# Performance work log

Hardware: AMD Instinct MI355X
Metric: run time of the kernel (lower is better)

## Reference

```python
import jax, jax.numpy as jnp
import numpy as np

B, S, D, H = 4, 2048, 1024, 16
HD = D // H
FF = 4 * D
EPS = 1e-5


def _layer_norm(x, w, b):
    mu = jnp.mean(x, axis=-1, keepdims=True)
    var = jnp.mean(jnp.square(x - mu), axis=-1, keepdims=True)
    return (x - mu) * jax.lax.rsqrt(var + EPS) * w + b


def setup_inputs() -> dict:
    key = jax.random.key(0)
    ks = jax.random.split(key, 8)
    std = 0.02
    return {
        "x": jax.random.normal(ks[0], (B, S, D), dtype=jnp.float32),
        "ln1_w": jnp.ones((D,), jnp.float32),
        "ln1_b": jnp.zeros((D,), jnp.float32),
        "w_qkv": jax.random.normal(ks[1], (D, 3 * D), dtype=jnp.float32) * std,  # fused QKV, no bias
        "w_proj": jax.random.normal(ks[2], (D, D), dtype=jnp.float32) * std,
        "b_proj": jnp.zeros((D,), jnp.float32),
        "ln2_w": jnp.ones((D,), jnp.float32),
        "ln2_b": jnp.zeros((D,), jnp.float32),
        "w_ff1": jax.random.normal(ks[3], (D, FF), dtype=jnp.float32) * std,
        "b_ff1": jnp.zeros((FF,), jnp.float32),
        "w_ff2": jax.random.normal(ks[4], (FF, D), dtype=jnp.float32) * std,
        "b_ff2": jnp.zeros((D,), jnp.float32),
    }


def reference(x, ln1_w, ln1_b, w_qkv, w_proj, b_proj, ln2_w, ln2_b, w_ff1, b_ff1, w_ff2, b_ff2):
    b, s, d = x.shape
    # --- attention branch (pre-LN) ---
    h = _layer_norm(x, ln1_w, ln1_b)
    kqv = (h @ w_qkv).reshape(b, s, H, HD, 3)  # fused projection, split by last index
    k, q, v = kqv[..., 0], kqv[..., 1], kqv[..., 2]  # each [b, s, H, HD]
    scores = jnp.einsum("bqhd,bkhd->bhqk", q, k) * (HD ** -0.5)  # [b,H,s,s]
    causal = jnp.tril(jnp.ones((s, s), dtype=bool))
    scores = jnp.where(causal, scores, -jnp.inf)
    weights = jax.nn.softmax(scores, axis=-1)
    ctx = jnp.einsum("bhqk,bkhd->bqhd", weights, v).reshape(b, s, d)
    attn_out = ctx @ w_proj + b_proj
    x = x + attn_out
    # --- feed-forward branch (pre-LN) ---
    h = _layer_norm(x, ln2_w, ln2_b)
    ff = jax.nn.gelu(h @ w_ff1 + b_ff1, approximate=False) @ w_ff2 + b_ff2
    return x + ff
```

## Files before the change

kernel.cpp:

```cpp
#include <hip/hip_runtime.h>

typedef unsigned short u16;
typedef unsigned int u32;
typedef __bf16 bf16x8 __attribute__((ext_vector_type(8)));
typedef float f32x4 __attribute__((ext_vector_type(4)));
typedef float f32x16 __attribute__((ext_vector_type(16)));
typedef unsigned short us8 __attribute__((ext_vector_type(8)));
typedef unsigned short us4 __attribute__((ext_vector_type(4)));
typedef unsigned int u32x4 __attribute__((ext_vector_type(4)));

#define B_ 4
#define S_ 2048
#define D_ 1024
#define H_ 16
#define HD_ 64
#define EPS_ 1e-5f
#define SCALE_ (0.125f * 1.44269504088896341f)
#define THR_ 3.0f

__device__ __forceinline__ u16 f2bf(float f) {
  unsigned u = __builtin_bit_cast(unsigned, f);
  u = (u + 0x7FFFu + ((u >> 16) & 1u)) >> 16;
  return (u16)u;
}

__device__ __forceinline__ float gelu_f(float x) {
  float u = x * (2.3022388f + 0.10294971f * x * x);
  float te = __builtin_amdgcn_exp2f(u);
  return x - x * __builtin_amdgcn_rcpf(1.0f + te);
}

typedef const __attribute__((address_space(1))) unsigned int* gp1;
typedef __attribute__((address_space(3))) unsigned int* lp3;
__device__ __forceinline__ void gl_lds16(const void* g, void* l) {
  __builtin_amdgcn_global_load_lds((gp1)(unsigned long long)g,
                                   (lp3)(unsigned int)(unsigned long long)l,
                                   16, 0, 0);
}

__device__ __forceinline__ u32 cvtpk_bf16(float lo, float hi) {
  u32 d;
  asm("v_cvt_pk_bf16_f32 %0, %1, %2" : "=v"(d) : "v"(lo), "v"(hi));
  return d;
}
__device__ __forceinline__ void swap32(u32& a, u32& b) {
  asm("v_permlane32_swap_b32 %0, %1" : "+v"(a), "+v"(b));
}

__device__ __forceinline__ f32x16 zero16() {
  f32x16 z;
#pragma unroll
  for (int i = 0; i < 16; i++) z[i] = 0.f;
  return z;
}

__global__ __launch_bounds__(256) void wconv_kernel(const float* __restrict__ W,
                                                    u16* __restrict__ Wt,
                                                    int Kd, int N) {
  __shared__ u16 tile[32][33];
  int bid = blockIdx.x;
  int nbn = N >> 5;
  int tk = bid / nbn, tn = bid % nbn;
  int tx = threadIdx.x & 31, ty = threadIdx.x >> 5;
#pragma unroll
  for (int i = 0; i < 4; i++) {
    int r = ty + i * 8;
    tile[r][tx] = f2bf(W[(size_t)(tk * 32 + r) * N + tn * 32 + tx]);
  }
  __syncthreads();
#pragma unroll
  for (int i = 0; i < 4; i++) {
    int r = ty + i * 8;
    Wt[(size_t)(tn * 32 + r) * Kd + tk * 32 + tx] = tile[tx][r];
  }
}

__global__ __launch_bounds__(256) void vtrans_kernel(const u16* __restrict__ Vc,
                                                     u16* __restrict__ Vt) {
  __shared__ u16 tile[64][72];
  int bh = blockIdx.x >> 5;
  int sb = blockIdx.x & 31;
  const u16* src = Vc + ((size_t)bh * S_ + sb * 64) * HD_;
  int r = threadIdx.x >> 2, c0 = (threadIdx.x & 3) * 16;
  *(us8*)&tile[r][c0] = *(const us8*)(src + r * HD_ + c0);
  *(us8*)&tile[r][c0 + 8] = *(const us8*)(src + r * HD_ + c0 + 8);
  __syncthreads();
  u16* dst = Vt + (size_t)bh * HD_ * S_ + sb * 64;
  int hd = threadIdx.x >> 2;
  int s0 = (threadIdx.x & 3) * 16;
  us8 a, b;
#pragma unroll
  for (int j = 0; j < 8; j++) a[j] = tile[s0 + j][hd];
#pragma unroll
  for (int j = 0; j < 8; j++) b[j] = tile[s0 + 8 + j][hd];
  *(us8*)(dst + (size_t)hd * S_ + s0) = a;
  *(us8*)(dst + (size_t)hd * S_ + s0 + 8) = b;
}

__global__ __launch_bounds__(256) void ln_kernel(const float* __restrict__ x,
                                                 const float* __restrict__ w,
                                                 const float* __restrict__ b,
                                                 u16* __restrict__ out) {
  int row = blockIdx.x;
  int t = threadIdx.x;
  int lane = t & 63, wid = t >> 6;
  const float4* xr = (const float4*)(x + (size_t)row * D_);
  float4 v = xr[t];
  float s = v.x + v.y + v.z + v.w;
  float q = v.x * v.x + v.y * v.y + v.z * v.z + v.w * v.w;
#pragma unroll
  for (int off = 1; off < 64; off <<= 1) {
    s += __shfl_xor(s, off);
    q += __shfl_xor(q, off);
  }
  __shared__ float red[8];
  if (lane == 0) { red[wid] = s; red[4 + wid] = q; }
  __syncthreads();
  s = red[0] + red[1] + red[2] + red[3];
  q = red[4] + red[5] + red[6] + red[7];
  float mu = s * (1.0f / D_);
  float var = q * (1.0f / D_) - mu * mu;
  float rs = rsqrtf(var + EPS_);
  int c = t * 4;
  float4 wv = *(const float4*)(w + c);
  float4 bv = *(const float4*)(b + c);
  us4 o;
  o[0] = f2bf((v.x - mu) * rs * wv.x + bv.x);
  o[1] = f2bf((v.y - mu) * rs * wv.y + bv.y);
  o[2] = f2bf((v.z - mu) * rs * wv.z + bv.z);
  o[3] = f2bf((v.w - mu) * rs * wv.w + bv.w);
  *(us4*)(out + (size_t)row * D_ + c) = o;
}

template <int MODE, int BM>
__global__ __launch_bounds__(512) void gemm256_kernel(
    const u16* __restrict__ A, const u16* __restrict__ Bt,
    const float* __restrict__ bias, const float* __restrict__ res,
    float* __restrict__ Cf, u16* __restrict__ Cb,
    u16* __restrict__ Qc, u16* __restrict__ Kc, u16* __restrict__ Vc,
    int M, int N, int K) {
  constexpr int MFRAG = BM / 32;
  constexpr int MH = MFRAG / 2;
  constexpr int AR = BM / 64;
  constexpr int RR = AR + 4;
  extern __shared__ __align__(16) u16 sm[];
  u16* Al = sm;
  u16* Bl = sm + 2 * BM * 64;
  int t = threadIdx.x;
  int nbn = N >> 8;
  int nwg = gridDim.x;
  int cpx = nwg >> 3;
  int bid = (blockIdx.x % 8) * cpx + blockIdx.x / 8;
  int bm = bid / nbn, bn = bid % nbn;
  int lane = t & 63, wid = t >> 6;
  int wm = wid >> 2, wn = wid & 3;
  int lrow = lane & 15, lgr = lane >> 4;
  int sl7 = lrow & 7;
  const u16* Ab = A + (size_t)bm * BM * K;
  const u16* Bb = Bt + (size_t)bn * 256 * K;
  int srt = t >> 3;
  int ssc = (((t & 7) ^ (srt & 7)) << 3);
  const u16* Asrc = Ab + (size_t)srt * K + ssc;
  const u16* Bsrc = Bb + (size_t)srt * K + ssc;

  auto stage = [&](int kt, int bsel) {
    int k0 = kt * 64;
    u16* Ad = Al + bsel * (BM * 64) + t * 8;
    u16* Bd = Bl + bsel * (256 * 64) + t * 8;
#pragma unroll
    for (int a2 = 0; a2 < AR; a2++)
      gl_lds16(Asrc + (size_t)(a2 * 64) * K + k0, Ad + a2 * 4096);
#pragma unroll
    for (int b2 = 0; b2 < 4; b2++)
      gl_lds16(Bsrc + (size_t)(b2 * 64) * K + k0, Bd + b2 * 4096);
  };

  f32x4 acc[MFRAG][4] = {};
  int NT = K >> 6;
  stage(0, 0);
  for (int kt = 0; kt < NT; kt++) {
    int cur = kt & 1;
    if (kt + 1 < NT) {
      stage(kt + 1, cur ^ 1);
      if constexpr (RR == 8) asm volatile("s_waitcnt vmcnt(8)" ::: "memory");
      else                   asm volatile("s_waitcnt vmcnt(6)" ::: "memory");
    } else {
      asm volatile("s_waitcnt vmcnt(0)" ::: "memory");
    }
    __builtin_amdgcn_sched_barrier(0);
    __builtin_amdgcn_s_barrier();
    __builtin_amdgcn_sched_barrier(0);
    const u16* Ac = Al + cur * (BM * 64);
    const u16* Bc = Bl + cur * (256 * 64);
#pragma unroll
    for (int mq = 0; mq < 2; mq++) {
      bf16x8 af[2][MH];
#pragma unroll
      for (int ks = 0; ks < 2; ks++) {
        int slot = ((ks << 2) | lgr) ^ sl7;
#pragma unroll
        for (int mm = 0; mm < MH; mm++)
          af[ks][mm] = *(const bf16x8*)&Ac[(wm * (BM / 2) + (mq * MH + mm) * 16 + lrow) * 64 + slot * 8];
      }
#pragma unroll
      for (int nq = 0; nq < 2; nq++) {
        bf16x8 bfm[2][2];
#pragma unroll
        for (int ks = 0; ks < 2; ks++) {
          int slot = ((ks << 2) | lgr) ^ sl7;
#pragma unroll
          for (int nn = 0; nn < 2; nn++)
            bfm[ks][nn] = *(const bf16x8*)&Bc[(wn * 64 + (nq * 2 + nn) * 16 + lrow) * 64 + slot * 8];
        }
        __builtin_amdgcn_s_setprio(1);
#pragma unroll
        for (int mm = 0; mm < MH; mm++)
#pragma unroll
          for (int nn = 0; nn < 2; nn++) {
            int m = mq * MH + mm, n = nq * 2 + nn;
            acc[m][n] = __builtin_amdgcn_mfma_f32_16x16x32_bf16(af[0][mm], bfm[0][nn], acc[m][n], 0, 0, 0);
            acc[m][n] = __builtin_amdgcn_mfma_f32_16x16x32_bf16(af[1][mm], bfm[1][nn], acc[m][n], 0, 0, 0);
          }
        __builtin_amdgcn_s_setprio(0);
      }
    }
    __builtin_amdgcn_sched_barrier(0);
    __builtin_amdgcn_s_barrier();
    __builtin_amdgcn_sched_barrier(0);
  }
#pragma unroll
  for (int n = 0; n < 4; n++) {
    int col = bn * 256 + wn * 64 + n * 16 + lrow;
    float bv = (MODE & 1) ? bias[col] : 0.0f;
    if (MODE & 16) {
      int c = col % 3;
      int hd = (col / 3) & 63;
      int h = col / 192;
      u16* dst = (c == 0) ? Kc : (c == 1) ? Qc : Vc;
#pragma unroll
      for (int m = 0; m < MFRAG; m++)
#pragma unroll
        for (int r = 0; r < 4; r++) {
          int row = bm * BM + wm * (BM / 2) + m * 16 + lgr * 4 + r;
          int bb = row >> 11, sIdx = row & 2047;
          dst[(((size_t)(bb * H_ + h)) * S_ + sIdx) * HD_ + hd] = f2bf(acc[m][n][r]);
        }
    } else {
#pragma unroll
      for (int m = 0; m < MFRAG; m++)
#pragma unroll
        for (int r = 0; r < 4; r++) {
          int row = bm * BM + wm * (BM / 2) + m * 16 + lgr * 4 + r;
          float v = acc[m][n][r] + bv;
          if (MODE & 2) v = gelu_f(v);
          if (MODE & 4) v += res[(size_t)row * N + col];
          if (MODE & 8) Cb[(size_t)row * N + col] = f2bf(v);
          else          Cf[(size_t)row * N + col] = v;
        }
    }
  }
}

__device__ __forceinline__ void attn_softmax_update(
    f32x16* s, int NSUB_rt, float& mrun, float& lrun, f32x16 (&o)[2], int hi) {
  float pmax = -3.0e38f;
  for (int sub = 0; sub < NSUB_rt; sub++)
#pragma unroll
    for (int r = 0; r < 16; r++) pmax = fmaxf(pmax, s[sub][r]);
  pmax = fmaxf(pmax, __shfl_xor(pmax, 32));
  bool ok = (pmax * SCALE_ <= mrun + THR_);
  if (!__all(ok)) {
    float mnew = fmaxf(mrun, pmax * SCALE_);
    float corr = __builtin_amdgcn_exp2f(mrun - mnew);
    mrun = mnew;
    lrun *= corr;
#pragma unroll
    for (int r = 0; r < 16; r++) {
      float cr = __shfl(corr, ((r & 3) + 8 * (r >> 2)) + 4 * hi);
      o[0][r] *= cr;
      o[1][r] *= cr;
    }
  }
  float m = mrun;
  float lacc = 0.f;
  for (int sub = 0; sub < NSUB_rt; sub++)
#pragma unroll
    for (int r = 0; r < 16; r++) {
      float p = __builtin_amdgcn_exp2f(__builtin_fmaf(s[sub][r], SCALE_, -m));
      s[sub][r] = p;
      lacc += p;
    }
  lrun += lacc;
}

__device__ __forceinline__ void attn_pfrag(const f32x16& s, bf16x8& pa, bf16x8& pb) {
  u32 a0 = cvtpk_bf16(s[0], s[1]);
  u32 a1 = cvtpk_bf16(s[2], s[3]);
  u32 a2 = cvtpk_bf16(s[4], s[5]);
  u32 a3 = cvtpk_bf16(s[6], s[7]);
  swap32(a0, a2);
  swap32(a1, a3);
  u32 b0 = cvtpk_bf16(s[8], s[9]);
  u32 b1 = cvtpk_bf16(s[10], s[11]);
  u32 b2 = cvtpk_bf16(s[12], s[13]);
  u32 b3 = cvtpk_bf16(s[14], s[15]);
  swap32(b0, b2);
  swap32(b1, b3);
  u32x4 fa = {a0, a1, a2, a3};
  u32x4 fb = {b0, b1, b2, b3};
  pa = __builtin_bit_cast(bf16x8, fa);
  pb = __builtin_bit_cast(bf16x8, fb);
}

template <bool MASK>
__device__ __forceinline__ void attn_chunk_tail(
    const u16* __restrict__ Kh, const u16* __restrict__ Vh,
    const bf16x8 (&qf)[4], f32x16 (&o)[2],
    float& mrun, float& lrun, int kb, int qrow, int hi, int ln31) {
  f32x16 s[1];
  f32x16 z = zero16();
  __builtin_amdgcn_s_setprio(1);
#pragma unroll
  for (int ks = 0; ks < 4; ks++) {
    bf16x8 kfr = *(const bf16x8*)(Kh + (size_t)(kb + ln31) * HD_ + ks * 16 + hi * 8);
    z = __builtin_amdgcn_mfma_f32_32x32x16_bf16(kfr, qf[ks], z, 0, 0, 0);
  }
  __builtin_amdgcn_s_setprio(0);
  if (MASK) {
#pragma unroll
    for (int r = 0; r < 16; r++) {
      int key = kb + (r & 3) + 8 * (r >> 2) + 4 * hi;
      if (key > qrow) z[r] = -3.0e38f;
    }
  }
  s[0] = z;
  attn_softmax_update(s, 1, mrun, lrun, o, hi);
  bf16x8 pa, pb;
  attn_pfrag(s[0], pa, pb);
  __builtin_amdgcn_s_setprio(1);
#pragma unroll
  for (int ht = 0; ht < 2; ht++) {
    const u16* vb = Vh + (size_t)(ht * 32 + ln31) * S_ + kb + hi * 8;
    bf16x8 v1 = *(const bf16x8*)(vb);
    bf16x8 v2 = *(const bf16x8*)(vb + 16);
    o[ht] = __builtin_amdgcn_mfma_f32_32x32x16_bf16(pa, v1, o[ht], 0, 0, 0);
    o[ht] = __builtin_amdgcn_mfma_f32_32x32x16_bf16(pb, v2, o[ht], 0, 0, 0);
  }
  __builtin_amdgcn_s_setprio(0);
}

__global__ __launch_bounds__(512) void attn_kernel(const u16* __restrict__ Q,
                                                   const u16* __restrict__ Kk,
                                                   const u16* __restrict__ Vt,
                                                   u16* __restrict__ ctx) {
  __shared__ __align__(16) u16 Kl[2][64 * 64];
  __shared__ __align__(16) u16 Vl[2][64 * 64];
  int t = threadIdx.x;
  int lane = t & 63, wid = t >> 6;
  int qblk = 7 - (int)(blockIdx.x >> 6);
  int bh = blockIdx.x & 63;
  int b = bh >> 4, h = bh & 15;
  const u16* Qh = Q + (size_t)bh * S_ * HD_;
  const u16* Kh = Kk + (size_t)bh * S_ * HD_;
  const u16* Vh = Vt + (size_t)bh * HD_ * S_;
  int qb = qblk * 256;
  int qbase = qb + wid * 32;
  int ln31 = lane & 31, hi = lane >> 5;
  int qrow = qbase + ln31;
  int l7 = ln31 & 7;

  int srow = t >> 3;
  int sslot = (t & 7) ^ (srow & 7);
  const u16* Ksrc = Kh + (size_t)srow * HD_ + sslot * 8;
  const u16* Vsrc = Vh + (size_t)srow * S_ + sslot * 8;

  bf16x8 qf[4];
#pragma unroll
  for (int ks = 0; ks < 4; ks++)
    qf[ks] = *(const bf16x8*)(Qh + (size_t)qrow * HD_ + ks * 16 + hi * 8);

  f32x16 o[2] = {zero16(), zero16()};
  float mrun = -1.0e30f, lrun = 0.f;

  int nf64 = qbase >> 6;
  int NT = (qb >> 6) + 3;

  gl_lds16(Ksrc, &Kl[0][t * 8]);
  gl_lds16(Vsrc, &Vl[0][t * 8]);
  for (int kt = 0; kt < NT; kt++) {
    int cur = kt & 1;
    if (kt + 1 < NT) {
      int kb1 = (kt + 1) * 64;
      gl_lds16(Ksrc + (size_t)kb1 * HD_, &Kl[cur ^ 1][t * 8]);
      gl_lds16(Vsrc + kb1, &Vl[cur ^ 1][t * 8]);
      asm volatile("s_waitcnt vmcnt(2)" ::: "memory");
    } else {
      asm volatile("s_waitcnt vmcnt(0)" ::: "memory");
    }
    __builtin_amdgcn_sched_barrier(0);
    __builtin_amdgcn_s_barrier();
    __builtin_amdgcn_sched_barrier(0);
    if (kt < nf64) {
      const u16* Kc = &Kl[cur][0];
      const u16* Vc = &Vl[cur][0];
      f32x16 s[2];
#pragma unroll
      for (int sub = 0; sub < 2; sub++) {
        f32x16 z = zero16();
        __builtin_amdgcn_s_setprio(1);
#pragma unroll
        for (int ks = 0; ks < 4; ks++) {
          int kr = sub * 32 + ln31;
          int sl = (ks * 2 + hi) ^ l7;
          bf16x8 kfr = *(const bf16x8*)&Kc[kr * 64 + sl * 8];
          z = __builtin_amdgcn_mfma_f32_32x32x16_bf16(kfr, qf[ks], z, 0, 0, 0);
        }
        __builtin_amdgcn_s_setprio(0);
        s[sub] = z;
      }
      attn_softmax_update(s, 2, mrun, lrun, o, hi);
#pragma unroll
      for (int sub = 0; sub < 2; sub++) {
        bf16x8 pa, pb;
        attn_pfrag(s[sub], pa, pb);
        __builtin_amdgcn_s_setprio(1);
#pragma unroll
        for (int ht = 0; ht < 2; ht++) {
          int vr = ht * 32 + ln31;
          int s1 = (sub * 4 + hi) ^ (vr & 7);
          int s2 = (sub * 4 + hi + 2) ^ (vr & 7);
          bf16x8 v1 = *(const bf16x8*)&Vc[vr * 64 + s1 * 8];
          bf16x8 v2 = *(const bf16x8*)&Vc[vr * 64 + s2 * 8];
          o[ht] = __builtin_amdgcn_mfma_f32_32x32x16_bf16(pa, v1, o[ht], 0, 0, 0);
          o[ht] = __builtin_amdgcn_mfma_f32_32x32x16_bf16(pb, v2, o[ht], 0, 0, 0);
        }
        __builtin_amdgcn_s_setprio(0);
      }
    }
    __builtin_amdgcn_sched_barrier(0);
    __builtin_amdgcn_s_barrier();
    __builtin_amdgcn_sched_barrier(0);
  }

  if (qbase & 32)
    attn_chunk_tail<false>(Kh, Vh, qf, o, mrun, lrun, qbase - 32, qrow, hi, ln31);
  attn_chunk_tail<true>(Kh, Vh, qf, o, mrun, lrun, qbase, qrow, hi, ln31);

  float l = lrun + __shfl_xor(lrun, 32);
  float inv = 1.0f / l;
#pragma unroll
  for (int r = 0; r < 16; r++) {
    float invr = __shfl(inv, ((r & 3) + 8 * (r >> 2)) + 4 * hi);
    int q = qbase + (r & 3) + 8 * (r >> 2) + 4 * hi;
    size_t base = ((size_t)b * S_ + q) * D_ + h * HD_;
    ctx[base + ln31] = f2bf(o[0][r] * invr);
    ctx[base + 32 + ln31] = f2bf(o[1][r] * invr);
  }
}

extern "C" void kernel_launch(void* const* d_in, const int* in_sizes, int n_in,
                              void* d_out, int out_size, void* d_ws, size_t ws_size,
                              hipStream_t stream) {
  const float* x = (const float*)d_in[0];
  const float* ln1w = (const float*)d_in[1];
  const float* ln1b = (const float*)d_in[2];
  const float* wqkv = (const float*)d_in[3];
  const float* wproj = (const float*)d_in[4];
  const float* bproj = (const float*)d_in[5];
  const float* ln2w = (const float*)d_in[6];
  const float* ln2b = (const float*)d_in[7];
  const float* wff1 = (const float*)d_in[8];
  const float* bff1 = (const float*)d_in[9];
  const float* wff2 = (const float*)d_in[10];
  const float* bff2 = (const float*)d_in[11];

  char* ws = (char*)d_ws;
  u16* wqkvT = (u16*)(ws + 0);
  u16* wprojT = (u16*)(ws + 6291456);
  u16* wff1T = (u16*)(ws + 8388608);
  u16* wff2T = (u16*)(ws + 16777216);
  u16* h1 = (u16*)(ws + 25165824);
  u16* Vt = (u16*)(ws + 25165824);
  u16* Qc = (u16*)(ws + 41943040);
  u16* Kc = (u16*)(ws + 58720256);
  u16* Vc = (u16*)(ws + 75497472);
  u16* ctx = (u16*)(ws + 92274688);
  float* x1 = (float*)(ws + 109051904);
  u16* h2 = (u16*)(ws + 142606336);
  u16* g = (u16*)(ws + 25165824);
  float* outp = (float*)d_out;

  hipFuncSetAttribute((const void*)gemm256_kernel<16, 256>,
                      hipFuncAttributeMaxDynamicSharedMemorySize, 131072);
  hipFuncSetAttribute((const void*)gemm256_kernel<11, 256>,
                      hipFuncAttributeMaxDynamicSharedMemorySize, 131072);
  hipFuncSetAttribute((const void*)gemm256_kernel<5, 128>,
                      hipFuncAttributeMaxDynamicSharedMemorySize, 98304);

  wconv_kernel<<<(1024 / 32) * (3072 / 32), 256, 0, stream>>>(wqkv, wqkvT, 1024, 3072);
  wconv_kernel<<<(1024 / 32) * (1024 / 32), 256, 0, stream>>>(wproj, wprojT, 1024, 1024);
  wconv_kernel<<<(1024 / 32) * (4096 / 32), 256, 0, stream>>>(wff1, wff1T, 1024, 4096);
  wconv_kernel<<<(4096 / 32) * (1024 / 32), 256, 0, stream>>>(wff2, wff2T, 4096, 1024);

  ln_kernel<<<8192, 256, 0, stream>>>(x, ln1w, ln1b, h1);
  gemm256_kernel<16, 256><<<384, 512, 131072, stream>>>(h1, wqkvT, nullptr, nullptr,
                                                        nullptr, nullptr, Qc, Kc, Vc,
                                                        8192, 3072, 1024);
  vtrans_kernel<<<64 * 32, 256, 0, stream>>>(Vc, Vt);
  attn_kernel<<<8 * 64, 512, 0, stream>>>(Qc, Kc, Vt, ctx);
  gemm256_kernel<5, 128><<<256, 512, 98304, stream>>>(ctx, wprojT, bproj, x, x1, nullptr,
                                                      nullptr, nullptr, nullptr,
                                                      8192, 1024, 1024);
  ln_kernel<<<8192, 256, 0, stream>>>(x1, ln2w, ln2b, h2);
  gemm256_kernel<11, 256><<<512, 512, 131072, stream>>>(h2, wff1T, bff1, nullptr, nullptr, g,
                                                        nullptr, nullptr, nullptr,
                                                        8192, 4096, 1024);
  gemm256_kernel<5, 128><<<256, 512, 98304, stream>>>(g, wff2T, bff2, x1, outp, nullptr,
                                                      nullptr, nullptr, nullptr,
                                                      8192, 1024, 4096);
}
```

Measured before the change: 402.6 us.

## Replace 256-wide GEMM tiles with 128x128x32 tiles and higher occupancy

Rewrites the GEMM kernel to use 128x128 output tiles with a K-step of 32, 256 threads and static double-buffered LDS, targeting three blocks per CU. This replaces the large 256-column tiles that used up to 128KB of dynamic shared memory and 512 threads. The intent is more workgroups and better latency hiding through occupancy. The risk is lower data reuse per tile, more global and LDS traffic, and more barriers per unit of MFMA work.

```diff
diff --git a/kernel.cpp b/kernel.cpp
--- a/kernel.cpp
+++ b/kernel.cpp
@@ -132,105 +132,78 @@
   *(us4*)(out + (size_t)row * D_ + c) = o;
 }
 
-template <int MODE, int BM>
-__global__ __launch_bounds__(512) void gemm256_kernel(
+template <int MODE>
+__global__ __launch_bounds__(256, 3) void gemm_kernel(
     const u16* __restrict__ A, const u16* __restrict__ Bt,
     const float* __restrict__ bias, const float* __restrict__ res,
     float* __restrict__ Cf, u16* __restrict__ Cb,
     u16* __restrict__ Qc, u16* __restrict__ Kc, u16* __restrict__ Vc,
     int M, int N, int K) {
-  constexpr int MFRAG = BM / 32;
-  constexpr int MH = MFRAG / 2;
-  constexpr int AR = BM / 64;
-  constexpr int RR = AR + 4;
-  extern __shared__ __align__(16) u16 sm[];
-  u16* Al = sm;
-  u16* Bl = sm + 2 * BM * 64;
+  __shared__ __align__(16) u16 Al[2][128 * 32];
+  __shared__ __align__(16) u16 Bl[2][128 * 32];
   int t = threadIdx.x;
-  int nbn = N >> 8;
+  int nbn = N >> 7;
   int nwg = gridDim.x;
   int cpx = nwg >> 3;
   int bid = (blockIdx.x % 8) * cpx + blockIdx.x / 8;
   int bm = bid / nbn, bn = bid % nbn;
   int lane = t & 63, wid = t >> 6;
-  int wm = wid >> 2, wn = wid & 3;
+  int wm = wid >> 1, wn = wid & 1;
   int lrow = lane & 15, lgr = lane >> 4;
-  int sl7 = lrow & 7;
-  const u16* Ab = A + (size_t)bm * BM * K;
-  const u16* Bb = Bt + (size_t)bn * 256 * K;
-  int srt = t >> 3;
-  int ssc = (((t & 7) ^ (srt & 7)) << 3);
-  const u16* Asrc = Ab + (size_t)srt * K + ssc;
-  const u16* Bsrc = Bb + (size_t)srt * K + ssc;
-
-  auto stage = [&](int kt, int bsel) {
-    int k0 = kt * 64;
-    u16* Ad = Al + bsel * (BM * 64) + t * 8;
-    u16* Bd = Bl + bsel * (256 * 64) + t * 8;
-#pragma unroll
-    for (int a2 = 0; a2 < AR; a2++)
-      gl_lds16(Asrc + (size_t)(a2 * 64) * K + k0, Ad + a2 * 4096);
-#pragma unroll
-    for (int b2 = 0; b2 < 4; b2++)
-      gl_lds16(Bsrc + (size_t)(b2 * 64) * K + k0, Bd + b2 * 4096);
-  };
-
-  f32x4 acc[MFRAG][4] = {};
-  int NT = K >> 6;
-  stage(0, 0);
+  const u16* Ab = A + (size_t)bm * 128 * K;
+  const u16* Bb = Bt + (size_t)bn * 128 * K;
+  int srow = t >> 2;
+  int sslot = (t & 3) ^ (srow & 3);
+  const u16* Asrc = Ab + (size_t)srow * K + sslot * 8;
+  const u16* Bsrc = Bb + (size_t)srow * K + sslot * 8;
+  int rdslot = lgr ^ (lrow & 3);
+
+  f32x4 acc[4][4] = {};
+  int NT = K >> 5;
+  {
+    gl_lds16(Asrc, &Al[0][t * 8]);
+    gl_lds16(Asrc + (size_t)64 * K, &Al[0][2048 + t * 8]);
+    gl_lds16(Bsrc, &Bl[0][t * 8]);
+    gl_lds16(Bsrc + (size_t)64 * K, &Bl[0][2048 + t * 8]);
+  }
   for (int kt = 0; kt < NT; kt++) {
     int cur = kt & 1;
     if (kt + 1 < NT) {
-      stage(kt + 1, cur ^ 1);
-      if constexpr (RR == 8) asm volatile("s_waitcnt vmcnt(8)" ::: "memory");
-      else                   asm volatile("s_waitcnt vmcnt(6)" ::: "memory");
+      int k1 = (kt + 1) * 32;
+      u16* Ad = &Al[cur ^ 1][t * 8];
+      u16* Bd = &Bl[cur ^ 1][t * 8];
+      gl_lds16(Asrc + k1, Ad);
+      gl_lds16(Asrc + (size_t)64 * K + k1, Ad + 2048);
+      gl_lds16(Bsrc + k1, Bd);
+      gl_lds16(Bsrc + (size_t)64 * K + k1, Bd + 2048);
+      asm volatile("s_waitcnt vmcnt(4)" ::: "memory");
     } else {
       asm volatile("s_waitcnt vmcnt(0)" ::: "memory");
     }
     __builtin_amdgcn_sched_barrier(0);
     __builtin_amdgcn_s_barrier();
     __builtin_amdgcn_sched_barrier(0);
-    const u16* Ac = Al + cur * (BM * 64);
-    const u16* Bc = Bl + cur * (256 * 64);
-#pragma unroll
-    for (int mq = 0; mq < 2; mq++) {
-      bf16x8 af[2][MH];
-#pragma unroll
-      for (int ks = 0; ks < 2; ks++) {
-        int slot = ((ks << 2) | lgr) ^ sl7;
-#pragma unroll
-        for (int mm = 0; mm < MH; mm++)
-          af[ks][mm] = *(const bf16x8*)&Ac[(wm * (BM / 2) + (mq * MH + mm) * 16 + lrow) * 64 + slot * 8];
-      }
-#pragma unroll
-      for (int nq = 0; nq < 2; nq++) {
-        bf16x8 bfm[2][2];
-#pragma unroll
-        for (int ks = 0; ks < 2; ks++) {
-          int slot = ((ks << 2) | lgr) ^ sl7;
-#pragma unroll
-          for (int nn = 0; nn < 2; nn++)
-            bfm[ks][nn] = *(const bf16x8*)&Bc[(wn * 64 + (nq * 2 + nn) * 16 + lrow) * 64 + slot * 8];
-        }
-        __builtin_amdgcn_s_setprio(1);
-#pragma unroll
-        for (int mm = 0; mm < MH; mm++)
-#pragma unroll
-          for (int nn = 0; nn < 2; nn++) {
-            int m = mq * MH + mm, n = nq * 2 + nn;
-            acc[m][n] = __builtin_amdgcn_mfma_f32_16x16x32_bf16(af[0][mm], bfm[0][nn], acc[m][n], 0, 0, 0);
-            acc[m][n] = __builtin_amdgcn_mfma_f32_16x16x32_bf16(af[1][mm], bfm[1][nn], acc[m][n], 0, 0, 0);
-          }
-        __builtin_amdgcn_s_setprio(0);
-      }
-    }
+    bf16x8 af[4], bfr[4];
+#pragma unroll
+    for (int m = 0; m < 4; m++)
+      af[m] = *(const bf16x8*)&Al[cur][(wm * 64 + m * 16 + lrow) * 32 + rdslot * 8];
+#pragma unroll
+    for (int n = 0; n < 4; n++)
+      bfr[n] = *(const bf16x8*)&Bl[cur][(wn * 64 + n * 16 + lrow) * 32 + rdslot * 8];
+    __builtin_amdgcn_s_setprio(1);
+#pragma unroll
+    for (int m = 0; m < 4; m++)
+#pragma unroll
+      for (int n = 0; n < 4; n++)
+        acc[m][n] = __builtin_amdgcn_mfma_f32_16x16x32_bf16(af[m], bfr[n], acc[m][n], 0, 0, 0);
+    __builtin_amdgcn_s_setprio(0);
     __builtin_amdgcn_sched_barrier(0);
     __builtin_amdgcn_s_barrier();
     __builtin_amdgcn_sched_barrier(0);
   }
 #pragma unroll
   for (int n = 0; n < 4; n++) {
-    int col = bn * 256 + wn * 64 + n * 16 + lrow;
+    int col = bn * 128 + wn * 64 + n * 16 + lrow;
     float bv = (MODE & 1) ? bias[col] : 0.0f;
     if (MODE & 16) {
       int c = col % 3;
@@ -238,19 +211,19 @@
       int h = col / 192;
       u16* dst = (c == 0) ? Kc : (c == 1) ? Qc : Vc;
 #pragma unroll
-      for (int m = 0; m < MFRAG; m++)
+      for (int m = 0; m < 4; m++)
 #pragma unroll
         for (int r = 0; r < 4; r++) {
-          int row = bm * BM + wm * (BM / 2) + m * 16 + lgr * 4 + r;
+          int row = bm * 128 + wm * 64 + m * 16 + lgr * 4 + r;
           int bb = row >> 11, sIdx = row & 2047;
           dst[(((size_t)(bb * H_ + h)) * S_ + sIdx) * HD_ + hd] = f2bf(acc[m][n][r]);
         }
     } else {
 #pragma unroll
-      for (int m = 0; m < MFRAG; m++)
+      for (int m = 0; m < 4; m++)
 #pragma unroll
         for (int r = 0; r < 4; r++) {
-          int row = bm * BM + wm * (BM / 2) + m * 16 + lgr * 4 + r;
+          int row = bm * 128 + wm * 64 + m * 16 + lgr * 4 + r;
           float v = acc[m][n][r] + bv;
           if (MODE & 2) v = gelu_f(v);
           if (MODE & 4) v += res[(size_t)row * N + col];
@@ -490,32 +463,21 @@
   u16* g = (u16*)(ws + 25165824);
   float* outp = (float*)d_out;
 
-  hipFuncSetAttribute((const void*)gemm256_kernel<16, 256>,
-                      hipFuncAttributeMaxDynamicSharedMemorySize, 131072);
-  hipFuncSetAttribute((const void*)gemm256_kernel<11, 256>,
-                      hipFuncAttributeMaxDynamicSharedMemorySize, 131072);
-  hipFuncSetAttribute((const void*)gemm256_kernel<5, 128>,
-                      hipFuncAttributeMaxDynamicSharedMemorySize, 98304);
-
   wconv_kernel<<<(1024 / 32) * (3072 / 32), 256, 0, stream>>>(wqkv, wqkvT, 1024, 3072);
   wconv_kernel<<<(1024 / 32) * (1024 / 32), 256, 0, stream>>>(wproj, wprojT, 1024, 1024);
   wconv_kernel<<<(1024 / 32) * (4096 / 32), 256, 0, stream>>>(wff1, wff1T, 1024, 4096);
   wconv_kernel<<<(4096 / 32) * (1024 / 32), 256, 0, stream>>>(wff2, wff2T, 4096, 1024);
 
   ln_kernel<<<8192, 256, 0, stream>>>(x, ln1w, ln1b, h1);
-  gemm256_kernel<16, 256><<<384, 512, 131072, stream>>>(h1, wqkvT, nullptr, nullptr,
-                                                        nullptr, nullptr, Qc, Kc, Vc,
-                                                        8192, 3072, 1024);
+  gemm_kernel<16><<<1536, 256, 0, stream>>>(h1, wqkvT, nullptr, nullptr, nullptr, nullptr,
+                                            Qc, Kc, Vc, 8192, 3072, 1024);
   vtrans_kernel<<<64 * 32, 256, 0, stream>>>(Vc, Vt);
   attn_kernel<<<8 * 64, 512, 0, stream>>>(Qc, Kc, Vt, ctx);
-  gemm256_kernel<5, 128><<<256, 512, 98304, stream>>>(ctx, wprojT, bproj, x, x1, nullptr,
-                                                      nullptr, nullptr, nullptr,
-                                                      8192, 1024, 1024);
+  gemm_kernel<5><<<512, 256, 0, stream>>>(ctx, wprojT, bproj, x, x1, nullptr,
+                                          nullptr, nullptr, nullptr, 8192, 1024, 1024);
   ln_kernel<<<8192, 256, 0, stream>>>(x1, ln2w, ln2b, h2);
-  gemm256_kernel<11, 256><<<512, 512, 131072, stream>>>(h2, wff1T, bff1, nullptr, nullptr, g,
-                                                        nullptr, nullptr, nullptr,
-                                                        8192, 4096, 1024);
-  gemm256_kernel<5, 128><<<256, 512, 98304, stream>>>(g, wff2T, bff2, x1, outp, nullptr,
-                                                      nullptr, nullptr, nullptr,
-                                                      8192, 1024, 4096);
-}
+  gemm_kernel<11><<<2048, 256, 0, stream>>>(h2, wff1T, bff1, nullptr, nullptr, g,
+                                            nullptr, nullptr, nullptr, 8192, 4096, 1024);
+  gemm_kernel<5><<<512, 256, 0, stream>>>(g, wff2T, bff2, x1, outp, nullptr,
+                                          nullptr, nullptr, nullptr, 8192, 1024, 4096);
+}
```

Result: slower. 411.6 us (+2.2%).

## Restructure GEMM mainloop into four quadrant phases with interleaved prefetch and barriers

Applied to the files above, without the earlier changes.

The GEMM kernel now splits each k-tile into four quadrant phases (M-half by N-half). Each phase issues part of the next tile's global-to-LDS loads, waits on finer-grained vmcnt counters, and then runs its MFMAs, so loads overlap with compute more evenly. The warp-to-tile mapping changes so each wave covers a quarter of the M rows and 32 columns per N-half. This adds more s_barrier calls per k-tile and makes the vmcnt accounting delicate, so a wrong count could cause a stall or a race.

```diff
diff --git a/kernel.cpp b/kernel.cpp
--- a/kernel.cpp
+++ b/kernel.cpp
@@ -132,24 +132,60 @@
   *(us4*)(out + (size_t)row * D_ + c) = o;
 }
 
+#define VWAIT(n)                                              \
+  do {                                                        \
+    asm volatile("s_waitcnt vmcnt(" #n ")" ::: "memory");     \
+    __builtin_amdgcn_sched_barrier(0);                        \
+  } while (0)
+
+#define GPH(MQ, NQ, STAGEOP, WAITOP)                                           \
+  {                                                                            \
+    const u16* Ac = sm + cur * (ASZ + BSZ);                                    \
+    const u16* Bc = Ac + ASZ;                                                  \
+    bf16x8 af[2][MH];                                                          \
+    bf16x8 bfm[2][2];                                                          \
+    _Pragma("unroll") for (int ks = 0; ks < 2; ks++) {                         \
+      int slot = ((((ks << 2) | lgr) ^ sl7)) * 8;                              \
+      _Pragma("unroll") for (int m = 0; m < MH; m++)                           \
+        af[ks][m] = *(const bf16x8*)&Ac[(MQ * (BM / 2) + wm * (BM / 4) +       \
+                                         m * 16 + lrow) * 64 + slot];          \
+      _Pragma("unroll") for (int nn = 0; nn < 2; nn++)                         \
+        bfm[ks][nn] = *(const bf16x8*)&Bc[(NQ * 128 + wn * 32 + nn * 16 +      \
+                                           lrow) * 64 + slot];                 \
+    }                                                                          \
+    STAGEOP;                                                                   \
+    WAITOP;                                                                    \
+    __builtin_amdgcn_s_barrier();                                              \
+    asm volatile("s_waitcnt lgkmcnt(0)" ::: "memory");                         \
+    __builtin_amdgcn_sched_barrier(0);                                         \
+    __builtin_amdgcn_s_setprio(1);                                             \
+    _Pragma("unroll") for (int m = 0; m < MH; m++)                             \
+      _Pragma("unroll") for (int nn = 0; nn < 2; nn++) {                       \
+        acc[MQ][NQ][m][nn] = __builtin_amdgcn_mfma_f32_16x16x32_bf16(          \
+            af[0][m], bfm[0][nn], acc[MQ][NQ][m][nn], 0, 0, 0);                \
+        acc[MQ][NQ][m][nn] = __builtin_amdgcn_mfma_f32_16x16x32_bf16(          \
+            af[1][m], bfm[1][nn], acc[MQ][NQ][m][nn], 0, 0, 0);                \
+      }                                                                        \
+    __builtin_amdgcn_s_setprio(0);                                             \
+    __builtin_amdgcn_s_barrier();                                              \
+    __builtin_amdgcn_sched_barrier(0);                                         \
+  }
+
 template <int MODE, int BM>
-__global__ __launch_bounds__(512) void gemm256_kernel(
+__global__ __launch_bounds__(512) void gemm8p_kernel(
     const u16* __restrict__ A, const u16* __restrict__ Bt,
     const float* __restrict__ bias, const float* __restrict__ res,
     float* __restrict__ Cf, u16* __restrict__ Cb,
     u16* __restrict__ Qc, u16* __restrict__ Kc, u16* __restrict__ Vc,
     int M, int N, int K) {
-  constexpr int MFRAG = BM / 32;
-  constexpr int MH = MFRAG / 2;
-  constexpr int AR = BM / 64;
-  constexpr int RR = AR + 4;
+  constexpr int LA = BM / 128;
+  constexpr int MH = BM / 64;
+  constexpr int ASZ = BM * 64;
+  constexpr int BSZ = 256 * 64;
   extern __shared__ __align__(16) u16 sm[];
-  u16* Al = sm;
-  u16* Bl = sm + 2 * BM * 64;
   int t = threadIdx.x;
   int nbn = N >> 8;
-  int nwg = gridDim.x;
-  int cpx = nwg >> 3;
+  int nwg = gridDim.x, cpx = nwg >> 3;
   int bid = (blockIdx.x % 8) * cpx + blockIdx.x / 8;
   int bm = bid / nbn, bn = bid % nbn;
   int lane = t & 63, wid = t >> 6;
@@ -163,100 +199,88 @@
   const u16* Asrc = Ab + (size_t)srt * K + ssc;
   const u16* Bsrc = Bb + (size_t)srt * K + ssc;
 
-  auto stage = [&](int kt, int bsel) {
+  auto stageA = [&](int kt, int bsel, int h) {
     int k0 = kt * 64;
-    u16* Ad = Al + bsel * (BM * 64) + t * 8;
-    u16* Bd = Bl + bsel * (256 * 64) + t * 8;
-#pragma unroll
-    for (int a2 = 0; a2 < AR; a2++)
-      gl_lds16(Asrc + (size_t)(a2 * 64) * K + k0, Ad + a2 * 4096);
-#pragma unroll
-    for (int b2 = 0; b2 < 4; b2++)
-      gl_lds16(Bsrc + (size_t)(b2 * 64) * K + k0, Bd + b2 * 4096);
+    u16* dst = sm + bsel * (ASZ + BSZ) + (h * (BM / 2)) * 64 + t * 8;
+#pragma unroll
+    for (int a = 0; a < LA; a++)
+      gl_lds16(Asrc + (size_t)(h * (BM / 2) + a * 64) * K + k0, dst + a * 4096);
   };
-
-  f32x4 acc[MFRAG][4] = {};
+  auto stageB = [&](int kt, int bsel, int h) {
+    int k0 = kt * 64;
+    u16* dst = sm + bsel * (ASZ + BSZ) + ASZ + (h * 128) * 64 + t * 8;
+#pragma unroll
+    for (int b2 = 0; b2 < 2; b2++)
+      gl_lds16(Bsrc + (size_t)(h * 128 + b2 * 64) * K + k0, dst + b2 * 4096);
+  };
+
+  f32x4 acc[2][2][MH][2] = {};
   int NT = K >> 6;
-  stage(0, 0);
-  for (int kt = 0; kt < NT; kt++) {
-    int cur = kt & 1;
-    if (kt + 1 < NT) {
-      stage(kt + 1, cur ^ 1);
-      if constexpr (RR == 8) asm volatile("s_waitcnt vmcnt(8)" ::: "memory");
-      else                   asm volatile("s_waitcnt vmcnt(6)" ::: "memory");
+  stageA(0, 0, 0);
+  stageB(0, 0, 0);
+  stageA(0, 0, 1);
+  stageB(0, 0, 1);
+  if constexpr (BM == 256) VWAIT(4); else VWAIT(3);
+  __builtin_amdgcn_s_barrier();
+  __builtin_amdgcn_sched_barrier(0);
+  for (int kt = 0; kt < NT - 1; kt++) {
+    int cur = kt & 1, nb = cur ^ 1;
+    if constexpr (BM == 256) {
+      GPH(0, 0, stageA(kt + 1, nb, 0), VWAIT(4));
+      GPH(1, 0, stageB(kt + 1, nb, 0), VWAIT(4));
+      GPH(0, 1, stageA(kt + 1, nb, 1), (void)0);
+      GPH(1, 1, stageB(kt + 1, nb, 1), VWAIT(4));
     } else {
-      asm volatile("s_waitcnt vmcnt(0)" ::: "memory");
-    }
-    __builtin_amdgcn_sched_barrier(0);
-    __builtin_amdgcn_s_barrier();
-    __builtin_amdgcn_sched_barrier(0);
-    const u16* Ac = Al + cur * (BM * 64);
-    const u16* Bc = Bl + cur * (256 * 64);
-#pragma unroll
-    for (int mq = 0; mq < 2; mq++) {
-      bf16x8 af[2][MH];
-#pragma unroll
-      for (int ks = 0; ks < 2; ks++) {
-        int slot = ((ks << 2) | lgr) ^ sl7;
-#pragma unroll
-        for (int mm = 0; mm < MH; mm++)
-          af[ks][mm] = *(const bf16x8*)&Ac[(wm * (BM / 2) + (mq * MH + mm) * 16 + lrow) * 64 + slot * 8];
+      GPH(0, 0, stageA(kt + 1, nb, 0), VWAIT(3));
+      GPH(1, 0, stageB(kt + 1, nb, 0), VWAIT(3));
+      GPH(0, 1, stageA(kt + 1, nb, 1), (void)0);
+      GPH(1, 1, stageB(kt + 1, nb, 1), VWAIT(3));
+    }
+  }
+  {
+    int cur = (NT - 1) & 1;
+    GPH(0, 0, (void)0, VWAIT(2));
+    GPH(1, 0, (void)0, VWAIT(0));
+    GPH(0, 1, (void)0, (void)0);
+    GPH(1, 1, (void)0, (void)0);
+  }
+#pragma unroll
+  for (int nq = 0; nq < 2; nq++) {
+#pragma unroll
+    for (int nn = 0; nn < 2; nn++) {
+      int col = bn * 256 + nq * 128 + wn * 32 + nn * 16 + lrow;
+      float bv = (MODE & 1) ? bias[col] : 0.0f;
+      if (MODE & 16) {
+        int c = col % 3;
+        int hd = (col / 3) & 63;
+        int h = col / 192;
+        u16* dst = (c == 0) ? Kc : (c == 1) ? Qc : Vc;
+#pragma unroll
+        for (int mq = 0; mq < 2; mq++)
+#pragma unroll
+          for (int m = 0; m < MH; m++)
+#pragma unroll
+            for (int r = 0; r < 4; r++) {
+              int row = bm * BM + mq * (BM / 2) + wm * (BM / 4) + m * 16 + lgr * 4 + r;
+              int bb = row >> 11, sIdx = row & 2047;
+              dst[(((size_t)(bb * H_ + h)) * S_ + sIdx) * HD_ + hd] =
+                  f2bf(acc[mq][nq][m][nn][r]);
+            }
+      } else {
+#pragma unroll
+        for (int mq = 0; mq < 2; mq++)
+#pragma unroll
+          for (int m = 0; m < MH; m++)
+#pragma unroll
+            for (int r = 0; r < 4; r++) {
+              int row = bm * BM + mq * (BM / 2) + wm * (BM / 4) + m * 16 + lgr * 4 + r;
+              float v = acc[mq][nq][m][nn][r] + bv;
+              if (MODE & 2) v = gelu_f(v);
+              if (MODE & 4) v += res[(size_t)row * N + col];
+              if (MODE & 8) Cb[(size_t)row * N + col] = f2bf(v);
+              else          Cf[(size_t)row * N + col] = v;
+            }
       }
-#pragma unroll
-      for (int nq = 0; nq < 2; nq++) {
-        bf16x8 bfm[2][2];
-#pragma unroll
-        for (int ks = 0; ks < 2; ks++) {
-          int slot = ((ks << 2) | lgr) ^ sl7;
-#pragma unroll
-          for (int nn = 0; nn < 2; nn++)
-            bfm[ks][nn] = *(const bf16x8*)&Bc[(wn * 64 + (nq * 2 + nn) * 16 + lrow) * 64 + slot * 8];
-        }
-        __builtin_amdgcn_s_setprio(1);
-#pragma unroll
-        for (int mm = 0; mm < MH; mm++)
-#pragma unroll
-          for (int nn = 0; nn < 2; nn++) {
-            int m = mq * MH + mm, n = nq * 2 + nn;
-            acc[m][n] = __builtin_amdgcn_mfma_f32_16x16x32_bf16(af[0][mm], bfm[0][nn], acc[m][n], 0, 0, 0);
-            acc[m][n] = __builtin_amdgcn_mfma_f32_16x16x32_bf16(af[1][mm], bfm[1][nn], acc[m][n], 0, 0, 0);
-          }
-        __builtin_amdgcn_s_setprio(0);
-      }
-    }
-    __builtin_amdgcn_sched_barrier(0);
-    __builtin_amdgcn_s_barrier();
-    __builtin_amdgcn_sched_barrier(0);
-  }
-#pragma unroll
-  for (int n = 0; n < 4; n++) {
-    int col = bn * 256 + wn * 64 + n * 16 + lrow;
-    float bv = (MODE & 1) ? bias[col] : 0.0f;
-    if (MODE & 16) {
-      int c = col % 3;
-      int hd = (col / 3) & 63;
-      int h = col / 192;
-      u16* dst = (c == 0) ? Kc : (c == 1) ? Qc : Vc;
-#pragma unroll
-      for (int m = 0; m < MFRAG; m++)
-#pragma unroll
-        for (int r = 0; r < 4; r++) {
-          int row = bm * BM + wm * (BM / 2) + m * 16 + lgr * 4 + r;
-          int bb = row >> 11, sIdx = row & 2047;
-          dst[(((size_t)(bb * H_ + h)) * S_ + sIdx) * HD_ + hd] = f2bf(acc[m][n][r]);
-        }
-    } else {
-#pragma unroll
-      for (int m = 0; m < MFRAG; m++)
-#pragma unroll
-        for (int r = 0; r < 4; r++) {
-          int row = bm * BM + wm * (BM / 2) + m * 16 + lgr * 4 + r;
-          float v = acc[m][n][r] + bv;
-          if (MODE & 2) v = gelu_f(v);
-          if (MODE & 4) v += res[(size_t)row * N + col];
-          if (MODE & 8) Cb[(size_t)row * N + col] = f2bf(v);
-          else          Cf[(size_t)row * N + col] = v;
-        }
     }
   }
 }
@@ -490,11 +514,11 @@
   u16* g = (u16*)(ws + 25165824);
   float* outp = (float*)d_out;
 
-  hipFuncSetAttribute((const void*)gemm256_kernel<16, 256>,
+  hipFuncSetAttribute((const void*)gemm8p_kernel<16, 256>,
                       hipFuncAttributeMaxDynamicSharedMemorySize, 131072);
-  hipFuncSetAttribute((const void*)gemm256_kernel<11, 256>,
+  hipFuncSetAttribute((const void*)gemm8p_kernel<11, 256>,
                       hipFuncAttributeMaxDynamicSharedMemorySize, 131072);
-  hipFuncSetAttribute((const void*)gemm256_kernel<5, 128>,
+  hipFuncSetAttribute((const void*)gemm8p_kernel<5, 128>,
                       hipFuncAttributeMaxDynamicSharedMemorySize, 98304);
 
   wconv_kernel<<<(1024 / 32) * (3072 / 32), 256, 0, stream>>>(wqkv, wqkvT, 1024, 3072);
@@ -503,19 +527,19 @@
   wconv_kernel<<<(4096 / 32) * (1024 / 32), 256, 0, stream>>>(wff2, wff2T, 4096, 1024);
 
   ln_kernel<<<8192, 256, 0, stream>>>(x, ln1w, ln1b, h1);
-  gemm256_kernel<16, 256><<<384, 512, 131072, stream>>>(h1, wqkvT, nullptr, nullptr,
-                                                        nullptr, nullptr, Qc, Kc, Vc,
-                                                        8192, 3072, 1024);
+  gemm8p_kernel<16, 256><<<384, 512, 131072, stream>>>(h1, wqkvT, nullptr, nullptr,
+                                                       nullptr, nullptr, Qc, Kc, Vc,
+                                                       8192, 3072, 1024);
   vtrans_kernel<<<64 * 32, 256, 0, stream>>>(Vc, Vt);
   attn_kernel<<<8 * 64, 512, 0, stream>>>(Qc, Kc, Vt, ctx);
-  gemm256_kernel<5, 128><<<256, 512, 98304, stream>>>(ctx, wprojT, bproj, x, x1, nullptr,
-                                                      nullptr, nullptr, nullptr,
-                                                      8192, 1024, 1024);
+  gemm8p_kernel<5, 128><<<256, 512, 98304, stream>>>(ctx, wprojT, bproj, x, x1, nullptr,
+                                                     nullptr, nullptr, nullptr,
+                                                     8192, 1024, 1024);
   ln_kernel<<<8192, 256, 0, stream>>>(x1, ln2w, ln2b, h2);
-  gemm256_kernel<11, 256><<<512, 512, 131072, stream>>>(h2, wff1T, bff1, nullptr, nullptr, g,
-                                                        nullptr, nullptr, nullptr,
-                                                        8192, 4096, 1024);
-  gemm256_kernel<5, 128><<<256, 512, 98304, stream>>>(g, wff2T, bff2, x1, outp, nullptr,
-                                                      nullptr, nullptr, nullptr,
-                                                      8192, 1024, 4096);
-}
+  gemm8p_kernel<11, 256><<<512, 512, 131072, stream>>>(h2, wff1T, bff1, nullptr, nullptr, g,
+                                                       nullptr, nullptr, nullptr,
+                                                       8192, 4096, 1024);
+  gemm8p_kernel<5, 128><<<256, 512, 98304, stream>>>(g, wff2T, bff2, x1, outp, nullptr,
+                                                     nullptr, nullptr, nullptr,
+                                                     8192, 1024, 4096);
+}
```

Result: no change. 395.9 us (-1.6%).
